# Kernel optimization log

Measured on AMD Instinct MI355X. Metric: run time of the kernel, lower is better.

Reference implementation:

```python
import jax, jax.numpy as jnp
import numpy as np

B, T, V, E, U = 64, 512, 32000, 1024, 1024


def setup_inputs() -> dict:
    key = jax.random.key(0)
    k0, k1, k2, k3 = jax.random.split(key, 4)
    x = jax.random.randint(k0, (B, T), 0, V, dtype=jnp.int32)
    hidden = jnp.zeros((B, U), jnp.float32)
    emb = jax.random.normal(k1, (V, E), jnp.float32) * 0.02
    Wx = jax.random.normal(k2, (E, 3 * U), jnp.float32) / np.sqrt(E).astype(np.float32)
    Wh = jax.random.normal(k3, (U, 3 * U), jnp.float32) / np.sqrt(U).astype(np.float32)
    b_i = jnp.zeros((3 * U,), jnp.float32)  # input bias (reset_after=True has 2 biases)
    b_r = jnp.zeros((3 * U,), jnp.float32)  # recurrent bias
    return {"x": x, "hidden": hidden, "emb": emb, "Wx": Wx, "Wh": Wh, "b_i": b_i, "b_r": b_r}


def reference(x, hidden, emb, Wx, Wh, b_i, b_r):
    # Embedding with mask_zero=True: mask = (token != 0)
    mask = (x != 0)                                   # [B,T]
    e = jnp.take(emb, x, axis=0)                      # [B,T,E]
    # Precompute all input projections in one big GEMM (z|r|h gate order, Keras layout)
    xp = jnp.einsum('bte,eu->btu', e, Wx) + b_i       # [B,T,3U]
    xp_t = jnp.moveaxis(xp, 1, 0)                     # [T,B,3U] time-major for scan
    m_t = jnp.moveaxis(mask, 1, 0)[..., None]         # [T,B,1]

    def step(h, inp):
        xpt, m = inp
        hp = h @ Wh + b_r                             # [B,3U]
        xz, xr, xh = jnp.split(xpt, 3, axis=-1)
        hz, hr, hh = jnp.split(hp, 3, axis=-1)
        z = jax.nn.sigmoid(xz + hz)
        r = jax.nn.sigmoid(xr + hr)
        cand = jnp.tanh(xh + r * hh)                  # reset_after=True: r applied post-matmul
        h_new = z * h + (1.0 - z) * cand
        h_new = jnp.where(m, h_new, h)                # masked steps copy state through
        return h_new, h_new

    state, out_t = jax.lax.scan(step, hidden, (xp_t, m_t))
    output = jnp.moveaxis(out_t, 0, 1)                # [B,T,U]
    return output, state
```

## Files before the change

### kernel.cpp

```cpp
#include <hip/hip_runtime.h>
#include <stdint.h>


#define B_SZ   64
#define T_LEN  512
#define U_DIM  1024
#define E_DIM  1024
#define G3     3072
#define BU     (B_SZ * U_DIM)
#define XP_SCALE 131072.0f
#define XP_INV   (1.0f / 131072.0f)
#define H_SCALE  32768.0f
#define H_INV    (1.0f / 32768.0f)
#define LDT    40
#define NWG    256

typedef unsigned short ushort_t;
typedef __attribute__((ext_vector_type(8))) short bf16x8;
typedef __attribute__((ext_vector_type(4))) float f32x4;

__device__ __forceinline__ ushort_t f2bf(float f) {
  unsigned u = __builtin_bit_cast(unsigned, f);
  u += 0x7fffu + ((u >> 16) & 1u);
  return (ushort_t)(u >> 16);
}
__device__ __forceinline__ float bf2f(ushort_t h) {
  return __builtin_bit_cast(float, (unsigned)h << 16);
}

__device__ __forceinline__ bf16x8 ldg_cohere_b128(const void* p) {
  bf16x8 r;
  asm volatile("global_load_dwordx4 %0, %1, off sc0 sc1"
               : "=v"(r) : "v"(p) : "memory");
  return r;
}
__device__ __forceinline__ void stg_cohere_u16(short* p, unsigned v) {
  asm volatile("global_store_short %0, %1, off sc0 sc1"
               :: "v"(p), "v"(v) : "memory");
}
__device__ __forceinline__ void stg_cohere_u32(unsigned* p, unsigned v) {
  asm volatile("global_store_dword %0, %1, off sc0 sc1"
               :: "v"(p), "v"(v) : "memory");
}
__device__ __forceinline__ unsigned ldg_cohere_u32(const unsigned* p) {
  unsigned r;
  asm volatile("global_load_dword %0, %1, off sc0 sc1\n\ts_waitcnt vmcnt(0)"
               : "=v"(r) : "v"(p) : "memory");
  return r;
}
__device__ __forceinline__ int ldg_sshort(const short* p) {
  int r;
  asm volatile("global_load_sshort %0, %1, off"
               : "=v"(r) : "v"(p) : "memory");
  return r;
}
__device__ __forceinline__ int ldg_s32(const int* p) {
  int r;
  asm volatile("global_load_dword %0, %1, off"
               : "=v"(r) : "v"(p) : "memory");
  return r;
}
__device__ __forceinline__ void stg_u32(float* p, float v) {
  asm volatile("global_store_dword %0, %1, off"
               :: "v"(p), "v"(v) : "memory");
}
#define WAITV(n) do { asm volatile("s_waitcnt vmcnt(" #n ")" ::: "memory"); \
                      __builtin_amdgcn_sched_barrier(0); } while (0)

__global__ __launch_bounds__(256) void gemm_xp(
    const float* __restrict__ emb,
    const float* __restrict__ Wx,
    const int* __restrict__ x,
    const float* __restrict__ b_i,
    short* __restrict__ xp)
{
  __shared__ ushort_t aH[128 * LDT];
  __shared__ ushort_t bH[128 * LDT];
  const int tid = threadIdx.x, lane = tid & 63, w = tid >> 6;
  const int bx = blockIdx.x;
  const int nIdx = bx % 24, mIdx = bx / 24;
  const int m0 = mIdx * 128, n0 = nIdx * 128;

  const int aRow0 = tid >> 2, aRow1 = (tid + 256) >> 2, aKoct = tid & 3;
  const size_t aBase0 = (size_t)x[m0 + aRow0] * E_DIM + (size_t)aKoct * 8;
  const size_t aBase1 = (size_t)x[m0 + aRow1] * E_DIM + (size_t)aKoct * 8;
  const int bN = tid & 127, bKoct0 = tid >> 7;

  const int wr = (w >> 1) * 64, wc = (w & 1) * 64;
  f32x4 acc[4][4];
#pragma unroll
  for (int i = 0; i < 4; i++)
#pragma unroll
    for (int j = 0; j < 4; j++) acc[i][j] = (f32x4){0.f, 0.f, 0.f, 0.f};

  for (int k0 = 0; k0 < E_DIM; k0 += 32) {
    __syncthreads();
#pragma unroll
    for (int pp = 0; pp < 2; ++pp) {
      const float* src = emb + (pp ? aBase1 : aBase0) + k0;
      int row = pp ? aRow1 : aRow0;
      float4 v0 = *(const float4*)(src);
      float4 v1 = *(const float4*)(src + 4);
      float vv[8] = {v0.x, v0.y, v0.z, v0.w, v1.x, v1.y, v1.z, v1.w};
      bf16x8 oh;
#pragma unroll
      for (int j = 0; j < 8; ++j) oh[j] = (short)f2bf(vv[j]);
      *(bf16x8*)&aH[row * LDT + aKoct * 8] = oh;
    }
#pragma unroll
    for (int kk = 0; kk < 2; ++kk) {
      int koct = bKoct0 + 2 * kk;
      float vv[8];
#pragma unroll
      for (int e = 0; e < 8; ++e)
        vv[e] = Wx[(size_t)(k0 + koct * 8 + e) * G3 + n0 + bN];
      bf16x8 oh;
#pragma unroll
      for (int j = 0; j < 8; ++j) oh[j] = (short)f2bf(vv[j]);
      *(bf16x8*)&bH[bN * LDT + koct * 8] = oh;
    }
    __syncthreads();
    bf16x8 afH[4], bfH[4];
#pragma unroll
    for (int mi = 0; mi < 4; mi++) {
      int off = (wr + mi * 16 + (lane & 15)) * LDT + (lane >> 4) * 8;
      afH[mi] = *(const bf16x8*)&aH[off];
    }
#pragma unroll
    for (int ni = 0; ni < 4; ni++) {
      int off = (wc + ni * 16 + (lane & 15)) * LDT + (lane >> 4) * 8;
      bfH[ni] = *(const bf16x8*)&bH[off];
    }
#pragma unroll
    for (int mi = 0; mi < 4; mi++)
#pragma unroll
      for (int ni = 0; ni < 4; ni++)
        acc[mi][ni] = __builtin_amdgcn_mfma_f32_16x16x32_bf16(afH[mi], bfH[ni], acc[mi][ni], 0, 0, 0);
  }
#pragma unroll
  for (int ni = 0; ni < 4; ni++) {
    int col = n0 + wc + ni * 16 + (lane & 15);
    float bias = b_i[col];
#pragma unroll
    for (int mi = 0; mi < 4; mi++) {
      int rbase = m0 + wr + mi * 16 + (lane >> 4) * 4;
#pragma unroll
      for (int i = 0; i < 4; i++) {
        int m = rbase + i;
        int b = m >> 9, t = m & 511;
        float v = acc[mi][ni][i] + bias;
        int q = __float2int_rn(v * XP_SCALE);
        q = q > 32767 ? 32767 : (q < -32768 ? -32768 : q);
        xp[(size_t)(t * 64 + b) * G3 + col] = (short)q;
      }
    }
  }
}

__global__ __launch_bounds__(256) void init_h(
    const float* __restrict__ hidden,
    short* __restrict__ h16,
    unsigned* __restrict__ flags)
{
  const int i = blockIdx.x * 256 + threadIdx.x;
  if (blockIdx.x < 16) flags[blockIdx.x * 256 + threadIdx.x] = 0u;
  if (i < BU) {
    int q = __float2int_rn(hidden[i] * H_SCALE);
    q = q > 32767 ? 32767 : (q < -32768 ? -32768 : q);
    h16[i] = (short)q;
  }
}

__global__ __launch_bounds__(512) void gru_scan(
    const float* __restrict__ hidden,
    const float* __restrict__ Wh,
    const float* __restrict__ b_r,
    const short* __restrict__ xp,
    const int* __restrict__ x,
    short* __restrict__ h16,
    unsigned* __restrict__ flags,
    float* __restrict__ out)
{
  __shared__ float part[8][3][64][4];
  __shared__ unsigned ready;
  const int tid  = threadIdx.x;
  const int lane = tid & 63;
  const int w    = tid >> 6;
  const int bx   = (int)blockIdx.x;
  const int uj   = bx & 63, bi = bx >> 6;
  const int u0   = uj * 16, b0 = bi * 16;
  const int c16  = lane & 15;
  const int kg   = lane >> 4;
  unsigned* gflags = flags + bi * 1024;
  const unsigned* pollp = gflags + lane * 16;

  bf16x8 BH[4][3], BL[4][3];
#pragma unroll
  for (int ks = 0; ks < 4; ++ks)
#pragma unroll
    for (int g = 0; g < 3; ++g) {
      bf16x8 bh, bl;
#pragma unroll
      for (int j = 0; j < 8; ++j) {
        int k = w * 128 + ks * 32 + kg * 8 + j;
        float v = Wh[(size_t)k * G3 + g * 1024 + u0 + c16];
        ushort_t hi = f2bf(v);
        bh[j] = (short)hi;
        bl[j] = (short)f2bf(v - bf2f(hi));
      }
      BH[ks][g] = bh;
      BL[ks][g] = bl;
    }

  const bool epi = (tid < 256);
  const int ebl = (tid >> 4) & 15, eul = tid & 15;
  const int eb = b0 + ebl, eu = u0 + eul;
  float brz = 0.f, brr = 0.f, brh = 0.f, hp = 0.f;
  if (epi) {
    brz = b_r[eu]; brr = b_r[1024 + eu]; brh = b_r[2048 + eu];
    hp  = hidden[(size_t)eb * U_DIM + eu];
  }

  asm volatile("s_waitcnt vmcnt(0) lgkmcnt(0)" ::: "memory");

  int xq0 = 0, xq1 = 0, xq2 = 0, xtok = 0;
  if (epi) {
    xq0 = ldg_sshort(xp + (size_t)eb * G3 + eu);
    xq1 = ldg_sshort(xp + (size_t)eb * G3 + 1024 + eu);
    xq2 = ldg_sshort(xp + (size_t)eb * G3 + 2048 + eu);
    xtok = ldg_s32(x + eb * T_LEN + 0);
  }

  unsigned spins = 0;
  for (int t = 0; t < T_LEN; ++t) {
    const short* __restrict__ rP = h16 + (size_t)(t & 1) * BU;
    short* __restrict__ wP       = h16 + (size_t)((t + 1) & 1) * BU;

    if (t > 0) {
      if (w == 0) {
        if (ready == 0u) {
          const unsigned tgt = (unsigned)t;
          while (spins < (1u << 22)) {
            unsigned f = ldg_cohere_u32(pollp);
            if (__ballot(f >= tgt) == ~0ull) break;
            __builtin_amdgcn_s_sleep(1);
            ++spins;
          }
        }
      }
      __syncthreads();
    }

    const short* pP = rP + (size_t)(b0 + c16) * U_DIM + w * 128 + kg * 8;

    f32x4 acc[3];
#pragma unroll
    for (int g = 0; g < 3; ++g) acc[g] = (f32x4){0.f, 0.f, 0.f, 0.f};

    bf16x8 P0, P1, P2, P3;
    P0 = ldg_cohere_b128(pP + 0 * 32);
    P1 = ldg_cohere_b128(pP + 1 * 32);
    P2 = ldg_cohere_b128(pP + 2 * 32);
    P3 = ldg_cohere_b128(pP + 3 * 32);

#define UNPCK(P_, AH_, AL_) \
    { \
      _Pragma("unroll") \
      for (int j = 0; j < 8; ++j) { \
        float v = (float)(short)P_[j] * H_INV; \
        ushort_t hi = f2bf(v); \
        AH_[j] = (short)hi; \
        AL_[j] = (short)f2bf(v - bf2f(hi)); \
      } \
    }
#define COMP(AH_, AL_, ks_) \
    _Pragma("unroll") \
    for (int g = 0; g < 3; ++g) { \
      acc[g] = __builtin_amdgcn_mfma_f32_16x16x32_bf16(AH_, BH[ks_][g], acc[g], 0, 0, 0); \
      acc[g] = __builtin_amdgcn_mfma_f32_16x16x32_bf16(AH_, BL[ks_][g], acc[g], 0, 0, 0); \
      acc[g] = __builtin_amdgcn_mfma_f32_16x16x32_bf16(AL_, BH[ks_][g], acc[g], 0, 0, 0); \
    }
    bf16x8 AH, AL;
    WAITV(3);
    UNPCK(P0, AH, AL)
    COMP(AH, AL, 0)
    WAITV(2);
    UNPCK(P1, AH, AL)
    COMP(AH, AL, 1)
    WAITV(1);
    UNPCK(P2, AH, AL)
    COMP(AH, AL, 2)
    WAITV(0);
    UNPCK(P3, AH, AL)
    COMP(AH, AL, 3)
#undef UNPCK
#undef COMP

#pragma unroll
    for (int g = 0; g < 3; ++g)
      *(f32x4*)&part[w][g][lane][0] = acc[g];

    __syncthreads();

    if (epi) {
      const int pl = (ebl >> 2) * 16 + eul, pe = ebl & 3;
      float sz = 0.f, sr = 0.f, sh = 0.f;
#pragma unroll
      for (int s = 0; s < 8; ++s) {
        sz += part[s][0][pl][pe];
        sr += part[s][1][pl][pe];
        sh += part[s][2][pl][pe];
      }

      const float hz = sz + brz, hr = sr + brr, hhv = sh + brh;
      const float xz = (float)xq0 * XP_INV;
      const float xr = (float)xq1 * XP_INV;
      const float xh = (float)xq2 * XP_INV;
      const float z = 1.f / (1.f + __expf(-(xz + hz)));
      const float r = 1.f / (1.f + __expf(-(xr + hr)));
      const float ca = xh + r * hhv;
      const float cand = 1.f - 2.f / (__expf(2.f * ca) + 1.f);
      float hn = z * hp + (1.f - z) * cand;
      hn = (xtok != 0) ? hn : hp;
      hp = hn;

      int q = __float2int_rn(hn * H_SCALE);
      q = q > 32767 ? 32767 : (q < -32768 ? -32768 : q);
      stg_cohere_u16(wP + (size_t)eb * U_DIM + eu, (unsigned)q);
      stg_u32(&out[((size_t)eb * T_LEN + t) * U_DIM + eu], hn);

      const int tp = (t < T_LEN - 1) ? t + 1 : t;
      xq0 = ldg_sshort(xp + ((size_t)tp * B_SZ + eb) * G3 + eu);
      xq1 = ldg_sshort(xp + ((size_t)tp * B_SZ + eb) * G3 + 1024 + eu);
      xq2 = ldg_sshort(xp + ((size_t)tp * B_SZ + eb) * G3 + 2048 + eu);
      xtok = ldg_s32(x + eb * T_LEN + tp);
      WAITV(5);
    } else if (w == 7) {
      const unsigned tgt2 = (unsigned)(t + 1);
      unsigned ok = 0;
#pragma unroll
      for (int it = 0; it < 2; ++it) {
        if (!ok) {
          unsigned f = ldg_cohere_u32(pollp);
          if (__ballot(f >= tgt2) == ~0ull) ok = 1u;
        }
      }
      if (lane == 0) ready = ok;
    }

    __syncthreads();
    if (tid == 0)
      stg_cohere_u32(gflags + uj * 16, (unsigned)(t + 1));
    __builtin_amdgcn_sched_barrier(0);
  }

  if (epi)
    out[(size_t)B_SZ * T_LEN * U_DIM + (size_t)eb * U_DIM + eu] = hp;
}

extern "C" void kernel_launch(void* const* d_in, const int* in_sizes, int n_in,
                              void* d_out, int out_size, void* d_ws, size_t ws_size,
                              hipStream_t stream) {
  const int*   x      = (const int*)  d_in[0];
  const float* hidden = (const float*)d_in[1];
  const float* emb    = (const float*)d_in[2];
  const float* Wx     = (const float*)d_in[3];
  const float* Wh     = (const float*)d_in[4];
  const float* b_i    = (const float*)d_in[5];
  const float* b_r    = (const float*)d_in[6];
  float* out = (float*)d_out;

  const size_t XP_B = (size_t)T_LEN * B_SZ * G3 * 2;
  const size_t NEED = XP_B + 4 * (size_t)BU + 16384;
  if (ws_size < NEED) return;

  short*    xp    = (short*)d_ws;
  short*    h16   = (short*)((char*)d_ws + XP_B);
  unsigned* flags = (unsigned*)(h16 + 2 * (size_t)BU);

  init_h<<<BU / 256, 256, 0, stream>>>(hidden, h16, flags);
  gemm_xp<<<(32768 / 128) * (G3 / 128), 256, 0, stream>>>(emb, Wx, x, b_i, xp);
  gru_scan<<<NWG, 512, 0, stream>>>(hidden, Wh, b_r, xp, x, h16, flags, out);
}
```

Before: 2.634 ms.

## Replace flag-based step barrier with step-tagged hidden-state words polled directly

Each hidden-state element is stored as a 32-bit word that packs the step number in the high half with the quantized value in the low half. Consumers poll the data loads themselves until every tag matches the current step, which removes the separate flag array, the flag store, the extra polling wave and a block barrier per step. The partial-sum LDS buffer is double-buffered so the trailing __syncthreads can go. In exchange the hidden-state traffic doubles, and whole tiles are re-read while spinning.

After: 3.736 ms. 41.8% more time.

```diff
diff --git a/kernel.cpp b/kernel.cpp
--- a/kernel.cpp
+++ b/kernel.cpp
@@ -18,6 +18,7 @@
 typedef unsigned short ushort_t;
 typedef __attribute__((ext_vector_type(8))) short bf16x8;
 typedef __attribute__((ext_vector_type(4))) float f32x4;
+typedef __attribute__((ext_vector_type(4))) unsigned int u32x4;
 
 __device__ __forceinline__ ushort_t f2bf(float f) {
   unsigned u = __builtin_bit_cast(unsigned, f);
@@ -28,50 +29,35 @@
   return __builtin_bit_cast(float, (unsigned)h << 16);
 }
 
-__device__ __forceinline__ bf16x8 ldg_cohere_b128(const void* p) {
-  bf16x8 r;
+__device__ __forceinline__ u32x4 ld_mall_x4(const void* p) {
+  u32x4 r;
   asm volatile("global_load_dwordx4 %0, %1, off sc0 sc1"
                : "=v"(r) : "v"(p) : "memory");
   return r;
 }
-__device__ __forceinline__ void stg_cohere_u16(short* p, unsigned v) {
-  asm volatile("global_store_short %0, %1, off sc0 sc1"
-               :: "v"(p), "v"(v) : "memory");
-}
-__device__ __forceinline__ void stg_cohere_u32(unsigned* p, unsigned v) {
+__device__ __forceinline__ void st_mall_u32(unsigned* p, unsigned v) {
   asm volatile("global_store_dword %0, %1, off sc0 sc1"
                :: "v"(p), "v"(v) : "memory");
 }
-__device__ __forceinline__ unsigned ldg_cohere_u32(const unsigned* p) {
-  unsigned r;
-  asm volatile("global_load_dword %0, %1, off sc0 sc1\n\ts_waitcnt vmcnt(0)"
-               : "=v"(r) : "v"(p) : "memory");
-  return r;
-}
 __device__ __forceinline__ int ldg_sshort(const short* p) {
   int r;
-  asm volatile("global_load_sshort %0, %1, off"
-               : "=v"(r) : "v"(p) : "memory");
+  asm volatile("global_load_sshort %0, %1, off" : "=v"(r) : "v"(p) : "memory");
   return r;
 }
 __device__ __forceinline__ int ldg_s32(const int* p) {
   int r;
-  asm volatile("global_load_dword %0, %1, off"
-               : "=v"(r) : "v"(p) : "memory");
+  asm volatile("global_load_dword %0, %1, off" : "=v"(r) : "v"(p) : "memory");
   return r;
 }
-__device__ __forceinline__ void stg_u32(float* p, float v) {
-  asm volatile("global_store_dword %0, %1, off"
-               :: "v"(p), "v"(v) : "memory");
-}
-#define WAITV(n) do { asm volatile("s_waitcnt vmcnt(" #n ")" ::: "memory"); \
-                      __builtin_amdgcn_sched_barrier(0); } while (0)
+__device__ __forceinline__ void stg_f32(float* p, float v) {
+  asm volatile("global_store_dword %0, %1, off" :: "v"(p), "v"(v) : "memory");
+}
+#define WAITV0 do { asm volatile("s_waitcnt vmcnt(0)" ::: "memory"); \
+                    __builtin_amdgcn_sched_barrier(0); } while (0)
 
 __global__ __launch_bounds__(256) void gemm_xp(
-    const float* __restrict__ emb,
-    const float* __restrict__ Wx,
-    const int* __restrict__ x,
-    const float* __restrict__ b_i,
+    const float* __restrict__ emb, const float* __restrict__ Wx,
+    const int* __restrict__ x, const float* __restrict__ b_i,
     short* __restrict__ xp)
 {
   __shared__ ushort_t aH[128 * LDT];
@@ -159,15 +145,14 @@
 
 __global__ __launch_bounds__(256) void init_h(
     const float* __restrict__ hidden,
-    short* __restrict__ h16,
-    unsigned* __restrict__ flags)
+    unsigned* __restrict__ h32)
 {
   const int i = blockIdx.x * 256 + threadIdx.x;
-  if (blockIdx.x < 16) flags[blockIdx.x * 256 + threadIdx.x] = 0u;
   if (i < BU) {
     int q = __float2int_rn(hidden[i] * H_SCALE);
     q = q > 32767 ? 32767 : (q < -32768 ? -32768 : q);
-    h16[i] = (short)q;
+    h32[i] = (unsigned)(unsigned short)(short)q;
+    h32[BU + i] = 0xFFFF0000u;
   }
 }
 
@@ -177,12 +162,10 @@
     const float* __restrict__ b_r,
     const short* __restrict__ xp,
     const int* __restrict__ x,
-    short* __restrict__ h16,
-    unsigned* __restrict__ flags,
+    unsigned* __restrict__ h32,
     float* __restrict__ out)
 {
-  __shared__ float part[8][3][64][4];
-  __shared__ unsigned ready;
+  __shared__ float part[2][8][3][64][4];
   const int tid  = threadIdx.x;
   const int lane = tid & 63;
   const int w    = tid >> 6;
@@ -191,8 +174,6 @@
   const int u0   = uj * 16, b0 = bi * 16;
   const int c16  = lane & 15;
   const int kg   = lane >> 4;
-  unsigned* gflags = flags + bi * 1024;
-  const unsigned* pollp = gflags + lane * 16;
 
   bf16x8 BH[4][3], BL[4][3];
 #pragma unroll
@@ -215,6 +196,7 @@
   const bool epi = (tid < 256);
   const int ebl = (tid >> 4) & 15, eul = tid & 15;
   const int eb = b0 + ebl, eu = u0 + eul;
+  const int pl = (ebl >> 2) * 16 + eul, pe = ebl & 3;
   float brz = 0.f, brr = 0.f, brh = 0.f, hp = 0.f;
   if (epi) {
     brz = b_r[eu]; brr = b_r[1024 + eu]; brh = b_r[2048 + eu];
@@ -233,44 +215,48 @@
 
   unsigned spins = 0;
   for (int t = 0; t < T_LEN; ++t) {
-    const short* __restrict__ rP = h16 + (size_t)(t & 1) * BU;
-    short* __restrict__ wP       = h16 + (size_t)((t + 1) & 1) * BU;
-
-    if (t > 0) {
-      if (w == 0) {
-        if (ready == 0u) {
-          const unsigned tgt = (unsigned)t;
-          while (spins < (1u << 22)) {
-            unsigned f = ldg_cohere_u32(pollp);
-            if (__ballot(f >= tgt) == ~0ull) break;
-            __builtin_amdgcn_s_sleep(1);
-            ++spins;
-          }
-        }
-      }
-      __syncthreads();
-    }
-
-    const short* pP = rP + (size_t)(b0 + c16) * U_DIM + w * 128 + kg * 8;
+    const unsigned* __restrict__ rP = h32 + (size_t)(t & 1) * BU;
+    unsigned* __restrict__ wP       = h32 + (size_t)((t + 1) & 1) * BU;
+
+    const unsigned* pP = rP + (size_t)(b0 + c16) * U_DIM + w * 128 + kg * 8;
+    const unsigned want = (unsigned)t << 16;
+
+    u32x4 Q0, Q1, Q2, Q3, Q4, Q5, Q6, Q7;
+    for (;;) {
+      Q0 = ld_mall_x4(pP + 0);   Q1 = ld_mall_x4(pP + 4);
+      Q2 = ld_mall_x4(pP + 32);  Q3 = ld_mall_x4(pP + 36);
+      Q4 = ld_mall_x4(pP + 64);  Q5 = ld_mall_x4(pP + 68);
+      Q6 = ld_mall_x4(pP + 96);  Q7 = ld_mall_x4(pP + 100);
+      WAITV0;
+      unsigned bad;
+#define CK(Q_) ((Q_[0] ^ want) | (Q_[1] ^ want) | (Q_[2] ^ want) | (Q_[3] ^ want))
+      bad = (CK(Q0) | CK(Q1) | CK(Q2) | CK(Q3) |
+             CK(Q4) | CK(Q5) | CK(Q6) | CK(Q7)) & 0xFFFF0000u;
+#undef CK
+      if (__ballot(bad == 0u) == ~0ull) break;
+      if (++spins > (1u << 20)) break;
+      if (spins > 2) __builtin_amdgcn_s_sleep(1);
+    }
 
     f32x4 acc[3];
 #pragma unroll
     for (int g = 0; g < 3; ++g) acc[g] = (f32x4){0.f, 0.f, 0.f, 0.f};
 
-    bf16x8 P0, P1, P2, P3;
-    P0 = ldg_cohere_b128(pP + 0 * 32);
-    P1 = ldg_cohere_b128(pP + 1 * 32);
-    P2 = ldg_cohere_b128(pP + 2 * 32);
-    P3 = ldg_cohere_b128(pP + 3 * 32);
-
-#define UNPCK(P_, AH_, AL_) \
+#define UNPK(QA_, QB_, AH_, AL_) \
     { \
       _Pragma("unroll") \
-      for (int j = 0; j < 8; ++j) { \
-        float v = (float)(short)P_[j] * H_INV; \
+      for (int j = 0; j < 4; ++j) { \
+        float v = (float)(short)(QA_[j] & 0xffffu) * H_INV; \
         ushort_t hi = f2bf(v); \
         AH_[j] = (short)hi; \
         AL_[j] = (short)f2bf(v - bf2f(hi)); \
+      } \
+      _Pragma("unroll") \
+      for (int j = 0; j < 4; ++j) { \
+        float v = (float)(short)(QB_[j] & 0xffffu) * H_INV; \
+        ushort_t hi = f2bf(v); \
+        AH_[4 + j] = (short)hi; \
+        AL_[4 + j] = (short)f2bf(v - bf2f(hi)); \
       } \
     }
 #define COMP(AH_, AL_, ks_) \
@@ -280,36 +266,33 @@
       acc[g] = __builtin_amdgcn_mfma_f32_16x16x32_bf16(AH_, BL[ks_][g], acc[g], 0, 0, 0); \
       acc[g] = __builtin_amdgcn_mfma_f32_16x16x32_bf16(AL_, BH[ks_][g], acc[g], 0, 0, 0); \
     }
-    bf16x8 AH, AL;
-    WAITV(3);
-    UNPCK(P0, AH, AL)
-    COMP(AH, AL, 0)
-    WAITV(2);
-    UNPCK(P1, AH, AL)
-    COMP(AH, AL, 1)
-    WAITV(1);
-    UNPCK(P2, AH, AL)
-    COMP(AH, AL, 2)
-    WAITV(0);
-    UNPCK(P3, AH, AL)
-    COMP(AH, AL, 3)
-#undef UNPCK
+    {
+      bf16x8 AH, AL;
+      UNPK(Q0, Q1, AH, AL)
+      COMP(AH, AL, 0)
+      UNPK(Q2, Q3, AH, AL)
+      COMP(AH, AL, 1)
+      UNPK(Q4, Q5, AH, AL)
+      COMP(AH, AL, 2)
+      UNPK(Q6, Q7, AH, AL)
+      COMP(AH, AL, 3)
+    }
+#undef UNPK
 #undef COMP
 
 #pragma unroll
     for (int g = 0; g < 3; ++g)
-      *(f32x4*)&part[w][g][lane][0] = acc[g];
+      *(f32x4*)&part[t & 1][w][g][lane][0] = acc[g];
 
     __syncthreads();
 
     if (epi) {
-      const int pl = (ebl >> 2) * 16 + eul, pe = ebl & 3;
       float sz = 0.f, sr = 0.f, sh = 0.f;
 #pragma unroll
       for (int s = 0; s < 8; ++s) {
-        sz += part[s][0][pl][pe];
-        sr += part[s][1][pl][pe];
-        sh += part[s][2][pl][pe];
+        sz += part[t & 1][s][0][pl][pe];
+        sr += part[t & 1][s][1][pl][pe];
+        sh += part[t & 1][s][2][pl][pe];
       }
 
       const float hz = sz + brz, hr = sr + brr, hhv = sh + brh;
@@ -326,31 +309,17 @@
 
       int q = __float2int_rn(hn * H_SCALE);
       q = q > 32767 ? 32767 : (q < -32768 ? -32768 : q);
-      stg_cohere_u16(wP + (size_t)eb * U_DIM + eu, (unsigned)q);
-      stg_u32(&out[((size_t)eb * T_LEN + t) * U_DIM + eu], hn);
+      const unsigned word = ((unsigned)(t + 1) << 16) |
+                            (unsigned)(unsigned short)(short)q;
+      st_mall_u32(wP + (size_t)eb * U_DIM + eu, word);
+      stg_f32(&out[((size_t)eb * T_LEN + t) * U_DIM + eu], hn);
 
       const int tp = (t < T_LEN - 1) ? t + 1 : t;
       xq0 = ldg_sshort(xp + ((size_t)tp * B_SZ + eb) * G3 + eu);
       xq1 = ldg_sshort(xp + ((size_t)tp * B_SZ + eb) * G3 + 1024 + eu);
       xq2 = ldg_sshort(xp + ((size_t)tp * B_SZ + eb) * G3 + 2048 + eu);
       xtok = ldg_s32(x + eb * T_LEN + tp);
-      WAITV(5);
-    } else if (w == 7) {
-      const unsigned tgt2 = (unsigned)(t + 1);
-      unsigned ok = 0;
-#pragma unroll
-      for (int it = 0; it < 2; ++it) {
-        if (!ok) {
-          unsigned f = ldg_cohere_u32(pollp);
-          if (__ballot(f >= tgt2) == ~0ull) ok = 1u;
-        }
-      }
-      if (lane == 0) ready = ok;
-    }
-
-    __syncthreads();
-    if (tid == 0)
-      stg_cohere_u32(gflags + uj * 16, (unsigned)(t + 1));
+    }
     __builtin_amdgcn_sched_barrier(0);
   }
 
@@ -371,14 +340,13 @@
   float* out = (float*)d_out;
 
   const size_t XP_B = (size_t)T_LEN * B_SZ * G3 * 2;
-  const size_t NEED = XP_B + 4 * (size_t)BU + 16384;
+  const size_t NEED = XP_B + 8 * (size_t)BU;
   if (ws_size < NEED) return;
 
-  short*    xp    = (short*)d_ws;
-  short*    h16   = (short*)((char*)d_ws + XP_B);
-  unsigned* flags = (unsigned*)(h16 + 2 * (size_t)BU);
-
-  init_h<<<BU / 256, 256, 0, stream>>>(hidden, h16, flags);
+  short*    xp  = (short*)d_ws;
+  unsigned* h32 = (unsigned*)((char*)d_ws + XP_B);
+
+  init_h<<<BU / 256, 256, 0, stream>>>(hidden, h32);
   gemm_xp<<<(32768 / 128) * (G3 / 128), 256, 0, stream>>>(emb, Wx, x, b_i, xp);
-  gru_scan<<<NWG, 512, 0, stream>>>(hidden, Wh, b_r, xp, x, h16, flags, out);
-}
+  gru_scan<<<NWG, 512, 0, stream>>>(hidden, Wh, b_r, xp, x, h32, out);
+}
```
